# Kernel tuning notes

Measured on AMD Instinct MI355X. Metric: run time of the kernel, lower is better.

## Reference

```python
import jax, jax.numpy as jnp
import numpy as np

D_MODEL = 768
N_HEADS = 12
D_K = D_MODEL // N_HEADS


def setup_inputs() -> dict:
    key = jax.random.key(0)
    ks = jax.random.split(key, 11)
    B, T = 4, 2048
    s = 1.0 / np.sqrt(D_K)
    so = 1.0 / np.sqrt(D_MODEL)
    return {
        "q": jax.random.normal(ks[0], (B, T, D_MODEL), jnp.float32),
        "k": jax.random.normal(ks[1], (B, T, D_MODEL), jnp.float32),
        "v": jax.random.normal(ks[2], (B, T, D_MODEL), jnp.float32),
        "Wq": jax.random.normal(ks[3], (D_K, D_K), jnp.float32) * s,
        "bq": jax.random.normal(ks[4], (D_K,), jnp.float32) * s,
        "Wk": jax.random.normal(ks[5], (D_K, D_K), jnp.float32) * s,
        "bk": jax.random.normal(ks[6], (D_K,), jnp.float32) * s,
        "Wv": jax.random.normal(ks[7], (D_K, D_K), jnp.float32) * s,
        "bv": jax.random.normal(ks[8], (D_K,), jnp.float32) * s,
        "Wo": jax.random.normal(ks[9], (D_MODEL, D_MODEL), jnp.float32) * so,
        "bo": jax.random.normal(ks[10], (D_MODEL,), jnp.float32) * so,
    }


def reference(q, k, v, Wq, bq, Wk, bk, Wv, bv, Wo, bo):
    B, T, _ = q.shape
    # split into heads: [B, T, H, d_k]; per-head Linear shares weights across heads
    qh = q.reshape(B, T, N_HEADS, D_K)
    kh = k.reshape(B, T, N_HEADS, D_K)
    vh = v.reshape(B, T, N_HEADS, D_K)
    # torch Linear: x @ W^T + b, then transpose to [B, H, T, d_k]
    qh = jnp.einsum("bthd,ed->bhte", qh, Wq) + bq
    kh = jnp.einsum("bthd,ed->bhte", kh, Wk) + bk
    vh = jnp.einsum("bthd,ed->bhte", vh, Wv) + bv
    # scaled dot-product attention, full [B,H,T,T] scores (faithful to source)
    scores = jnp.einsum("bhqd,bhkd->bhqk", qh, kh) / jnp.sqrt(
        jnp.asarray(D_K, qh.dtype)
    )
    attn = jax.nn.softmax(scores, axis=-1)
    # einsum 'ijkl,ijlr->ikjr' -> output laid out [B, T, H, d_k]
    out_h = jnp.einsum("bhqk,bhkd->bqhd", attn, vh)
    concat = out_h.reshape(B, T, D_MODEL)
    return concat @ Wo.T + bo
```

## Files before the change

### kernel.cpp

```cpp
#include <hip/hip_runtime.h>


#define T_SEQ  2048
#define NH     12
#define DK     64
#define DMODEL 768
#define BATCH  4

typedef __attribute__((ext_vector_type(8))) short short8;
typedef __attribute__((ext_vector_type(4))) float f32x4;
typedef __attribute__((ext_vector_type(4))) unsigned short us4;

#define CEXP (0.125f * 1.44269504088896340736f)

__device__ __forceinline__ unsigned cvt_pk_bf16(float lo, float hi) {
  unsigned r;
  asm("v_cvt_pk_bf16_f32 %0, %1, %2" : "=v"(r) : "v"(lo), "v"(hi));
  return r;
}
__device__ __forceinline__ unsigned short f2bf1(float f) {
  unsigned r;
  asm("v_cvt_pk_bf16_f32 %0, %1, %1" : "=v"(r) : "v"(f));
  return (unsigned short)r;
}
__device__ __forceinline__ us4 f4_to_bf4(float4 v) {
  union { unsigned u[2]; us4 r; } t;
  t.u[0] = cvt_pk_bf16(v.x, v.y);
  t.u[1] = cvt_pk_bf16(v.z, v.w);
  return t.r;
}


__global__ __launch_bounds__(256, 4)
void qkv_proj_kernel(const float* __restrict__ qin,
                     const float* __restrict__ kin,
                     const float* __restrict__ vin,
                     const float* __restrict__ Wq, const float* __restrict__ bq,
                     const float* __restrict__ Wk, const float* __restrict__ bk,
                     const float* __restrict__ Wv, const float* __restrict__ bv,
                     unsigned short* __restrict__ Qp,
                     unsigned short* __restrict__ Kp,
                     unsigned short* __restrict__ Vt)
{
  const int tt  = blockIdx.x;
  const int bh  = blockIdx.y;
  const int p   = blockIdx.z;
  const int b   = bh / NH, h = bh % NH;
  const int t0  = tt * 64;
  const int tid = threadIdx.x;
  const int wv  = tid >> 6;
  const int ln  = tid & 63;
  const int c   = ln & 15;
  const int qd  = ln >> 4;

  __shared__ __align__(16) unsigned short sX[64 * 72];
  __shared__ __align__(16) unsigned short sW[64 * 72];
  __shared__ __align__(16) unsigned short sVtr[64 * 68];

  const float* in = (p == 0) ? qin : (p == 1) ? kin : vin;
  const float* W  = (p == 0) ? Wq  : (p == 1) ? Wk  : Wv;
  const float* bs = (p == 0) ? bq  : (p == 1) ? bk  : bv;

  const int r0 = tid >> 4, g = tid & 15;
#pragma unroll
  for (int l = 0; l < 4; ++l) {
    int r = l * 16 + r0;
    float4 xv = *reinterpret_cast<const float4*>(in + ((size_t)(b * T_SEQ + t0 + r)) * DMODEL + h * DK + g * 4);
    *reinterpret_cast<us4*>(&sX[r * 72 + g * 4]) = f4_to_bf4(xv);
    float4 wvv = *reinterpret_cast<const float4*>(W + r * DK + g * 4);
    *reinterpret_cast<us4*>(&sW[r * 72 + g * 4]) = f4_to_bf4(wvv);
  }
  __syncthreads();

  short8 af[2];
#pragma unroll
  for (int kc = 0; kc < 2; ++kc)
    af[kc] = *reinterpret_cast<const short8*>(&sX[(wv * 16 + c) * 72 + kc * 32 + qd * 8]);

  f32x4 acc[4];
#pragma unroll
  for (int nb = 0; nb < 4; ++nb) {
    f32x4 a = {0.f, 0.f, 0.f, 0.f};
#pragma unroll
    for (int kc = 0; kc < 2; ++kc) {
      short8 bf = *reinterpret_cast<const short8*>(&sW[(nb * 16 + c) * 72 + kc * 32 + qd * 8]);
      a = __builtin_amdgcn_mfma_f32_16x16x32_bf16(af[kc], bf, a, 0, 0, 0);
    }
    acc[nb] = a;
  }

  if (p < 2) {
    unsigned short* outp = (p == 0) ? Qp : Kp;
    const float sc = (p == 0) ? CEXP : 1.0f;
#pragma unroll
    for (int nb = 0; nb < 4; ++nb) {
      int n = nb * 16 + c;
      float bias = bs[n] * sc;
#pragma unroll
      for (int r = 0; r < 4; ++r) {
        int t = t0 + wv * 16 + qd * 4 + r;
        outp[((size_t)bh * T_SEQ + t) * DK + n] = f2bf1(fmaf(acc[nb][r], sc, bias));
      }
    }
  } else {
#pragma unroll
    for (int nb = 0; nb < 4; ++nb) {
      int n = nb * 16 + c;
      float bias = bs[n];
#pragma unroll
      for (int r = 0; r < 4; ++r) {
        int row = wv * 16 + qd * 4 + r;
        sVtr[n * 68 + row] = f2bf1(acc[nb][r] + bias);
      }
    }
    __syncthreads();
#pragma unroll
    for (int l = 0; l < 4; ++l) {
      int d = l * 16 + r0;
      us4 val = *reinterpret_cast<const us4*>(&sVtr[d * 68 + g * 4]);
      *reinterpret_cast<us4*>(Vt + ((size_t)bh * DK + d) * T_SEQ + t0 + g * 4) = val;
    }
  }
}

__global__ __launch_bounds__(256, 3)
void flash_kernel(const unsigned short* __restrict__ Qp,
                  const unsigned short* __restrict__ Kp,
                  const unsigned short* __restrict__ Vt,
                  unsigned short* __restrict__ concat)
{
  const int lin = blockIdx.y * 16 + blockIdx.x;
  const int xcd = lin & 7;
  const int li  = lin >> 3;
  const int bh  = xcd * 6 + (li >> 4);
  const int qt  = li & 15;
  const int b   = bh / NH, h = bh % NH;
  const int tid = threadIdx.x;
  const int wv  = tid >> 6;
  const int ln  = tid & 63;
  const int c   = ln & 15;
  const int qd  = ln >> 4;

  __shared__ __align__(16) unsigned short sK[2][64 * 72];
  __shared__ __align__(16) unsigned short sV[2][64 * 72];

  const int row0 = qt * 128 + wv * 32;

  short8 qf[2][2];
#pragma unroll
  for (int f = 0; f < 2; ++f) {
    const unsigned short* qb = Qp + ((size_t)bh * T_SEQ + row0 + f * 16 + c) * DK + qd * 8;
    qf[f][0] = *reinterpret_cast<const short8*>(qb);
    qf[f][1] = *reinterpret_cast<const short8*>(qb + 32);
  }

  const int r0 = tid >> 4, g = tid & 15;
  us4 kreg[4], vreg[4];
#define LOAD_TILE(J)                                                                   \
  {                                                                                    \
    _Pragma("unroll")                                                                  \
    for (int l_ = 0; l_ < 4; ++l_) {                                                   \
      int r_ = l_ * 16 + r0;                                                           \
      kreg[l_] = *reinterpret_cast<const us4*>(Kp + ((size_t)bh * T_SEQ + (J) * 64 + r_) * DK + g * 4); \
      vreg[l_] = *reinterpret_cast<const us4*>(Vt + ((size_t)bh * DK + r_) * T_SEQ + (J) * 64 + g * 4); \
    }                                                                                  \
  }
#define WRITE_BUF(B)                                                                   \
  {                                                                                    \
    _Pragma("unroll")                                                                  \
    for (int l_ = 0; l_ < 4; ++l_) {                                                   \
      int r_ = l_ * 16 + r0;                                                           \
      *reinterpret_cast<us4*>(&sK[B][r_ * 72 + g * 4]) = kreg[l_];                     \
      *reinterpret_cast<us4*>(&sV[B][r_ * 72 + g * 4]) = vreg[l_];                     \
    }                                                                                  \
  }

  LOAD_TILE(0);
  WRITE_BUF(0);
  LOAD_TILE(1);

  f32x4 o[2][4];
  f32x4 lacc[2];
#pragma unroll
  for (int f = 0; f < 2; ++f) {
    lacc[f] = (f32x4){0.f, 0.f, 0.f, 0.f};
#pragma unroll
    for (int nb = 0; nb < 4; ++nb) o[f][nb] = (f32x4){0.f, 0.f, 0.f, 0.f};
  }

  short8 ones;
#pragma unroll
  for (int i = 0; i < 8; ++i) ones[i] = (short)0x3F80;

  for (int j = 0; j < T_SEQ / 64; ++j) {
    __syncthreads();
    const int cur = j & 1;
    WRITE_BUF((j + 1) & 1);
    LOAD_TILE((j + 2) & (T_SEQ / 64 - 1));

    short8 kf[4][2];
#pragma unroll
    for (int nb = 0; nb < 4; ++nb) {
      kf[nb][0] = *reinterpret_cast<const short8*>(&sK[cur][(nb * 16 + c) * 72 + qd * 8]);
      kf[nb][1] = *reinterpret_cast<const short8*>(&sK[cur][(nb * 16 + c) * 72 + 32 + qd * 8]);
    }

    short8 pf[2][2];
#pragma unroll
    for (int f = 0; f < 2; ++f) {
      f32x4 stf[4];
#pragma unroll
      for (int nb = 0; nb < 4; ++nb) {
        f32x4 a = {0.f, 0.f, 0.f, 0.f};
        a = __builtin_amdgcn_mfma_f32_16x16x32_bf16(kf[nb][0], qf[f][0], a, 0, 0, 0);
        a = __builtin_amdgcn_mfma_f32_16x16x32_bf16(kf[nb][1], qf[f][1], a, 0, 0, 0);
        stf[nb] = a;
      }
      unsigned pk[4][2];
#pragma unroll
      for (int nb = 0; nb < 4; ++nb) {
        float p0 = __builtin_amdgcn_exp2f(stf[nb][0]);
        float p1 = __builtin_amdgcn_exp2f(stf[nb][1]);
        float p2 = __builtin_amdgcn_exp2f(stf[nb][2]);
        float p3 = __builtin_amdgcn_exp2f(stf[nb][3]);
        pk[nb][0] = cvt_pk_bf16(p0, p1);
        pk[nb][1] = cvt_pk_bf16(p2, p3);
      }
#pragma unroll
      for (int kc = 0; kc < 2; ++kc) {
        union { unsigned w[4]; short8 s; } u;
#pragma unroll
        for (int pr = 0; pr < 2; ++pr) {
          unsigned X = pk[2 * kc][pr];
          unsigned Y = pk[2 * kc + 1][pr];
          auto s32 = __builtin_amdgcn_permlane32_swap(X, Y, false, false);
          auto s16 = __builtin_amdgcn_permlane16_swap(s32[0], s32[1], false, false);
          u.w[pr]     = s16[0];
          u.w[2 + pr] = s16[1];
        }
        pf[f][kc] = u.s;
      }
    }

    short8 vf[4][2];
#pragma unroll
    for (int nb = 0; nb < 4; ++nb) {
      vf[nb][0] = *reinterpret_cast<const short8*>(&sV[cur][(nb * 16 + c) * 72 + qd * 8]);
      vf[nb][1] = *reinterpret_cast<const short8*>(&sV[cur][(nb * 16 + c) * 72 + 32 + qd * 8]);
    }

#pragma unroll
    for (int f = 0; f < 2; ++f) {
      lacc[f] = __builtin_amdgcn_mfma_f32_16x16x32_bf16(pf[f][0], ones, lacc[f], 0, 0, 0);
      lacc[f] = __builtin_amdgcn_mfma_f32_16x16x32_bf16(pf[f][1], ones, lacc[f], 0, 0, 0);
    }

#pragma unroll
    for (int f = 0; f < 2; ++f)
#pragma unroll
      for (int nb = 0; nb < 4; ++nb) {
        o[f][nb] = __builtin_amdgcn_mfma_f32_16x16x32_bf16(pf[f][0], vf[nb][0], o[f][nb], 0, 0, 0);
        o[f][nb] = __builtin_amdgcn_mfma_f32_16x16x32_bf16(pf[f][1], vf[nb][1], o[f][nb], 0, 0, 0);
      }
  }

#pragma unroll
  for (int f = 0; f < 2; ++f) {
    float linv[4];
#pragma unroll
    for (int r = 0; r < 4; ++r) linv[r] = __builtin_amdgcn_rcpf(lacc[f][r]);
#pragma unroll
    for (int r = 0; r < 4; ++r) {
      int t = row0 + f * 16 + qd * 4 + r;
#pragma unroll
      for (int nb = 0; nb < 4; ++nb) {
        concat[((size_t)(b * T_SEQ + t)) * DMODEL + h * DK + nb * 16 + c] =
            f2bf1(o[f][nb][r] * linv[r]);
      }
    }
  }
#undef LOAD_TILE
#undef WRITE_BUF
}

__global__ __launch_bounds__(256, 3)
void oproj_kernel(const unsigned short* __restrict__ A,
                  const float* __restrict__ Wo,
                  const float* __restrict__ bo,
                  float* __restrict__ out)
{
  const int nt  = blockIdx.x;
  const int mt  = blockIdx.y;
  const int tid = threadIdx.x;
  const int wv  = tid >> 6;
  const int ln  = tid & 63;
  const int c   = ln & 15;
  const int qd  = ln >> 4;

  __shared__ __align__(16) unsigned short sA[128 * 72];
  __shared__ __align__(16) unsigned short sB[64 * 72];

  const int r0 = tid >> 4, g = tid & 15;
  us4 areg[8];
  float4 breg[4];
#define LOAD_K(KK)                                                                       \
  {                                                                                      \
    _Pragma("unroll")                                                                    \
    for (int l = 0; l < 8; ++l)                                                          \
      areg[l] = *reinterpret_cast<const us4*>(A + ((size_t)(mt * 128 + l * 16 + r0)) * DMODEL + (KK) * 64 + g * 4); \
    _Pragma("unroll")                                                                    \
    for (int l = 0; l < 4; ++l)                                                          \
      breg[l] = *reinterpret_cast<const float4*>(Wo + ((size_t)(nt * 64 + l * 16 + r0)) * DMODEL + (KK) * 64 + g * 4); \
  }

  LOAD_K(0);

  f32x4 acc[2][4];
#pragma unroll
  for (int f = 0; f < 2; ++f)
#pragma unroll
    for (int nb = 0; nb < 4; ++nb) acc[f][nb] = (f32x4){0.f, 0.f, 0.f, 0.f};

  for (int kk = 0; kk < DMODEL / 64; ++kk) {
    __syncthreads();
#pragma unroll
    for (int l = 0; l < 8; ++l)
      *reinterpret_cast<us4*>(&sA[(l * 16 + r0) * 72 + g * 4]) = areg[l];
#pragma unroll
    for (int l = 0; l < 4; ++l)
      *reinterpret_cast<us4*>(&sB[(l * 16 + r0) * 72 + g * 4]) = f4_to_bf4(breg[l]);
    __syncthreads();

    int kn = kk + 1 < DMODEL / 64 ? kk + 1 : 0;
    LOAD_K(kn);

    short8 af[2][2];
#pragma unroll
    for (int f = 0; f < 2; ++f) {
      af[f][0] = *reinterpret_cast<const short8*>(&sA[(wv * 32 + f * 16 + c) * 72 + qd * 8]);
      af[f][1] = *reinterpret_cast<const short8*>(&sA[(wv * 32 + f * 16 + c) * 72 + 32 + qd * 8]);
    }
#pragma unroll
    for (int nb = 0; nb < 4; ++nb) {
      short8 b0 = *reinterpret_cast<const short8*>(&sB[(nb * 16 + c) * 72 + qd * 8]);
      short8 b1 = *reinterpret_cast<const short8*>(&sB[(nb * 16 + c) * 72 + 32 + qd * 8]);
#pragma unroll
      for (int f = 0; f < 2; ++f) {
        acc[f][nb] = __builtin_amdgcn_mfma_f32_16x16x32_bf16(af[f][0], b0, acc[f][nb], 0, 0, 0);
        acc[f][nb] = __builtin_amdgcn_mfma_f32_16x16x32_bf16(af[f][1], b1, acc[f][nb], 0, 0, 0);
      }
    }
  }

#pragma unroll
  for (int f = 0; f < 2; ++f)
#pragma unroll
    for (int nb = 0; nb < 4; ++nb) {
      int n = nt * 64 + nb * 16 + c;
      float bias = bo[n];
#pragma unroll
      for (int r = 0; r < 4; ++r) {
        int m = mt * 128 + wv * 32 + f * 16 + qd * 4 + r;
        out[(size_t)m * DMODEL + n] = acc[f][nb][r] + bias;
      }
    }
#undef LOAD_K
}

extern "C" void kernel_launch(void* const* d_in, const int* in_sizes, int n_in,
                              void* d_out, int out_size, void* d_ws, size_t ws_size,
                              hipStream_t stream) {
  const float* q  = (const float*)d_in[0];
  const float* k  = (const float*)d_in[1];
  const float* v  = (const float*)d_in[2];
  const float* Wq = (const float*)d_in[3];
  const float* bq = (const float*)d_in[4];
  const float* Wk = (const float*)d_in[5];
  const float* bk = (const float*)d_in[6];
  const float* Wv = (const float*)d_in[7];
  const float* bv = (const float*)d_in[8];
  const float* Wo = (const float*)d_in[9];
  const float* bo = (const float*)d_in[10];

  const size_t NTOK = (size_t)BATCH * T_SEQ;
  const size_t PER  = NTOK * DK * NH;
  unsigned short* Qp     = (unsigned short*)d_ws;
  unsigned short* Kp     = Qp + PER;
  unsigned short* Vt     = Kp + PER;
  unsigned short* concat = Vt + PER;

  dim3 blk(256);
  qkv_proj_kernel<<<dim3(32, BATCH * NH, 3), blk, 0, stream>>>(q, k, v, Wq, bq, Wk, bk, Wv, bv, Qp, Kp, Vt);
  flash_kernel<<<dim3(16, BATCH * NH), blk, 0, stream>>>(Qp, Kp, Vt, concat);
  oproj_kernel<<<dim3(12, 64), blk, 0, stream>>>(concat, Wo, bo, (float*)d_out);
}
```

Measured before the change: 213.9 us.

## Process 128 tokens per QKV-projection block and stage Q/K stores through LDS

The QKV projection kernel now handles 128 tokens per block instead of 64, halving the grid and reusing each loaded weight tile and B-fragment across two row fragments. Q/K outputs are staged through shared memory (reusing the input buffer) and written as vectorized 8-byte stores instead of scattered 2-byte stores. The V transpose also reuses the input buffer. This cuts redundant weight loads and uncoalesced global writes, at the cost of an extra barrier and fewer, larger blocks.

Measured after the change: 213.7 us. No clear change (-0.1%).

```diff
diff --git a/kernel.cpp b/kernel.cpp
--- a/kernel.cpp
+++ b/kernel.cpp
@@ -46,16 +46,15 @@
   const int bh  = blockIdx.y;
   const int p   = blockIdx.z;
   const int b   = bh / NH, h = bh % NH;
-  const int t0  = tt * 64;
+  const int t0  = tt * 128;
   const int tid = threadIdx.x;
   const int wv  = tid >> 6;
   const int ln  = tid & 63;
   const int c   = ln & 15;
   const int qd  = ln >> 4;
 
-  __shared__ __align__(16) unsigned short sX[64 * 72];
+  __shared__ __align__(16) unsigned short sX[128 * 72];
   __shared__ __align__(16) unsigned short sW[64 * 72];
-  __shared__ __align__(16) unsigned short sVtr[64 * 68];
 
   const float* in = (p == 0) ? qin : (p == 1) ? kin : vin;
   const float* W  = (p == 0) ? Wq  : (p == 1) ? Wk  : Wv;
@@ -63,62 +62,87 @@
 
   const int r0 = tid >> 4, g = tid & 15;
 #pragma unroll
-  for (int l = 0; l < 4; ++l) {
+  for (int l = 0; l < 8; ++l) {
     int r = l * 16 + r0;
     float4 xv = *reinterpret_cast<const float4*>(in + ((size_t)(b * T_SEQ + t0 + r)) * DMODEL + h * DK + g * 4);
     *reinterpret_cast<us4*>(&sX[r * 72 + g * 4]) = f4_to_bf4(xv);
+  }
+#pragma unroll
+  for (int l = 0; l < 4; ++l) {
+    int r = l * 16 + r0;
     float4 wvv = *reinterpret_cast<const float4*>(W + r * DK + g * 4);
     *reinterpret_cast<us4*>(&sW[r * 72 + g * 4]) = f4_to_bf4(wvv);
   }
   __syncthreads();
 
-  short8 af[2];
-#pragma unroll
-  for (int kc = 0; kc < 2; ++kc)
-    af[kc] = *reinterpret_cast<const short8*>(&sX[(wv * 16 + c) * 72 + kc * 32 + qd * 8]);
-
-  f32x4 acc[4];
+  short8 af[2][2];
+#pragma unroll
+  for (int f = 0; f < 2; ++f)
+#pragma unroll
+    for (int kc = 0; kc < 2; ++kc)
+      af[f][kc] = *reinterpret_cast<const short8*>(&sX[(wv * 32 + f * 16 + c) * 72 + kc * 32 + qd * 8]);
+
+  f32x4 acc[2][4];
 #pragma unroll
   for (int nb = 0; nb < 4; ++nb) {
-    f32x4 a = {0.f, 0.f, 0.f, 0.f};
-#pragma unroll
-    for (int kc = 0; kc < 2; ++kc) {
-      short8 bf = *reinterpret_cast<const short8*>(&sW[(nb * 16 + c) * 72 + kc * 32 + qd * 8]);
-      a = __builtin_amdgcn_mfma_f32_16x16x32_bf16(af[kc], bf, a, 0, 0, 0);
-    }
-    acc[nb] = a;
-  }
+    short8 b0 = *reinterpret_cast<const short8*>(&sW[(nb * 16 + c) * 72 + qd * 8]);
+    short8 b1 = *reinterpret_cast<const short8*>(&sW[(nb * 16 + c) * 72 + 32 + qd * 8]);
+#pragma unroll
+    for (int f = 0; f < 2; ++f) {
+      f32x4 a = {0.f, 0.f, 0.f, 0.f};
+      a = __builtin_amdgcn_mfma_f32_16x16x32_bf16(af[f][0], b0, a, 0, 0, 0);
+      a = __builtin_amdgcn_mfma_f32_16x16x32_bf16(af[f][1], b1, a, 0, 0, 0);
+      acc[f][nb] = a;
+    }
+  }
+
+  __syncthreads();
 
   if (p < 2) {
     unsigned short* outp = (p == 0) ? Qp : Kp;
     const float sc = (p == 0) ? CEXP : 1.0f;
 #pragma unroll
-    for (int nb = 0; nb < 4; ++nb) {
-      int n = nb * 16 + c;
-      float bias = bs[n] * sc;
-#pragma unroll
-      for (int r = 0; r < 4; ++r) {
-        int t = t0 + wv * 16 + qd * 4 + r;
-        outp[((size_t)bh * T_SEQ + t) * DK + n] = f2bf1(fmaf(acc[nb][r], sc, bias));
-      }
+    for (int f = 0; f < 2; ++f)
+#pragma unroll
+      for (int nb = 0; nb < 4; ++nb) {
+        int n = nb * 16 + c;
+        float bias = bs[n] * sc;
+#pragma unroll
+        for (int r = 0; r < 4; ++r) {
+          int row = wv * 32 + f * 16 + qd * 4 + r;
+          sX[row * 68 + n] = f2bf1(fmaf(acc[f][nb][r], sc, bias));
+        }
+      }
+    __syncthreads();
+#pragma unroll
+    for (int l = 0; l < 8; ++l) {
+      int idx = l * 256 + tid;
+      int r  = idx >> 4;
+      int g2 = idx & 15;
+      us4 val = *reinterpret_cast<const us4*>(&sX[r * 68 + g2 * 4]);
+      *reinterpret_cast<us4*>(outp + ((size_t)bh * T_SEQ + t0 + r) * DK + g2 * 4) = val;
     }
   } else {
 #pragma unroll
-    for (int nb = 0; nb < 4; ++nb) {
-      int n = nb * 16 + c;
-      float bias = bs[n];
-#pragma unroll
-      for (int r = 0; r < 4; ++r) {
-        int row = wv * 16 + qd * 4 + r;
-        sVtr[n * 68 + row] = f2bf1(acc[nb][r] + bias);
-      }
-    }
+    for (int f = 0; f < 2; ++f)
+#pragma unroll
+      for (int nb = 0; nb < 4; ++nb) {
+        int n = nb * 16 + c;
+        float bias = bs[n];
+#pragma unroll
+        for (int r = 0; r < 4; ++r) {
+          int row = wv * 32 + f * 16 + qd * 4 + r;
+          sX[n * 136 + row] = f2bf1(acc[f][nb][r] + bias);
+        }
+      }
     __syncthreads();
 #pragma unroll
-    for (int l = 0; l < 4; ++l) {
-      int d = l * 16 + r0;
-      us4 val = *reinterpret_cast<const us4*>(&sVtr[d * 68 + g * 4]);
-      *reinterpret_cast<us4*>(Vt + ((size_t)bh * DK + d) * T_SEQ + t0 + g * 4) = val;
+    for (int l = 0; l < 8; ++l) {
+      int idx = l * 256 + tid;
+      int d  = idx >> 5;
+      int gg = idx & 31;
+      us4 val = *reinterpret_cast<const us4*>(&sX[d * 136 + gg * 4]);
+      *reinterpret_cast<us4*>(Vt + ((size_t)bh * DK + d) * T_SEQ + t0 + gg * 4) = val;
     }
   }
 }
@@ -390,7 +414,7 @@
   unsigned short* concat = Vt + PER;
 
   dim3 blk(256);
-  qkv_proj_kernel<<<dim3(32, BATCH * NH, 3), blk, 0, stream>>>(q, k, v, Wq, bq, Wk, bk, Wv, bv, Qp, Kp, Vt);
+  qkv_proj_kernel<<<dim3(16, BATCH * NH, 3), blk, 0, stream>>>(q, k, v, Wq, bq, Wk, bk, Wv, bv, Qp, Kp, Vt);
   flash_kernel<<<dim3(16, BATCH * NH), blk, 0, stream>>>(Qp, Kp, Vt, concat);
   oproj_kernel<<<dim3(12, 64), blk, 0, stream>>>(concat, Wo, bo, (float*)d_out);
 }
```
